# Kernel tuning notes

Hardware: AMD Instinct MI355X
Metric: run time of the kernel (lower is better)

## Reference

```python
import jax, jax.numpy as jnp
import numpy as np

N_NODES = 100000
N_EDGES = 1600000
N_GRAPHS = 1000
D_IN = 128
HID = 128
OUT = 6


def setup_inputs() -> dict:
    key = jax.random.key(0)
    ks = jax.random.split(key, 12)
    s = 1.0 / np.sqrt(HID)
    x = jax.random.normal(ks[0], (N_NODES, D_IN), dtype=jnp.float32)
    ei = jax.random.randint(ks[1], (2, N_EDGES), 0, N_NODES, dtype=jnp.int64)
    batch = jnp.sort(jax.random.randint(ks[2], (N_NODES,), 0, N_GRAPHS, dtype=jnp.int64))
    return {
        "x": x,
        "ei": ei,
        "batch": batch,
        "W1a": jax.random.normal(ks[3], (D_IN, HID), dtype=jnp.float32) * s,
        "b1a": jnp.zeros((HID,), jnp.float32),
        "W1b": jax.random.normal(ks[4], (HID, HID), dtype=jnp.float32) * s,
        "b1b": jnp.zeros((HID,), jnp.float32),
        "W2a": jax.random.normal(ks[5], (HID, HID), dtype=jnp.float32) * s,
        "b2a": jnp.zeros((HID,), jnp.float32),
        "W2b": jax.random.normal(ks[6], (HID, HID), dtype=jnp.float32) * s,
        "b2b": jnp.zeros((HID,), jnp.float32),
        "Wlin": jax.random.normal(ks[7], (HID, OUT), dtype=jnp.float32) * s,
        "blin": jnp.zeros((OUT,), jnp.float32),
    }


def _gin_conv(x, src, dst, Wa, ba, Wb, bb):
    # PyG GINConv (eps=0): mlp(x_i + sum_{j->i} x_j)
    agg = jax.ops.segment_sum(x[src], dst, num_segments=N_NODES)
    h = agg + x
    h = jnp.maximum(h @ Wa + ba, 0.0)
    return h @ Wb + bb


def reference(x, ei, batch, W1a, b1a, W1b, b1b, W2a, b2a, W2b, b2b, Wlin, blin):
    src, dst = ei[0], ei[1]
    h = jnp.maximum(_gin_conv(x, src, dst, W1a, b1a, W1b, b1b), 0.0)
    # dropout is identity in eval mode
    h = _gin_conv(h, src, dst, W2a, b2a, W2b, b2b)
    # global mean pool per graph
    sums = jax.ops.segment_sum(h, batch, num_segments=N_GRAPHS)
    cnts = jax.ops.segment_sum(jnp.ones((h.shape[0], 1), h.dtype), batch, num_segments=N_GRAPHS)
    pooled = sums / jnp.maximum(cnts, 1.0)
    return pooled @ Wlin + blin
```

## Files before the change

kernel.cpp:

```cpp
#include <hip/hip_runtime.h>

#define N_NODES 100000
#define N_EDGES 1600000
#define N_GRAPHS 1000
#define HID 128
#define OUTD 6

#define BUCK_LOG 7
#define BUCK_W (1 << BUCK_LOG)
#define NBUCK ((N_NODES + BUCK_W - 1) >> BUCK_LOG)
#define BCAP 4096
#define FILL_BLOCKS 512
#define FILL_CHUNK 3128

#define CVT_BLOCKS 6250
#define GST_BLOCKS 391
#define PACK_BLOCKS 32
#define PREP_BLOCKS (CVT_BLOCKS + GST_BLOCKS + PACK_BLOCKS + FILL_BLOCKS)

typedef _Float16 h2 __attribute__((ext_vector_type(2)));
typedef _Float16 half8 __attribute__((ext_vector_type(8)));
typedef float f32x4 __attribute__((ext_vector_type(4)));

__global__ __launch_bounds__(256) void k_prep(const float* __restrict__ x,
                                              const int* __restrict__ batch,
                                              const int* __restrict__ srcv,
                                              const int* __restrict__ dstv,
                                              const float* __restrict__ W1a,
                                              const float* __restrict__ W1b,
                                              const float* __restrict__ W2a,
                                              const float* __restrict__ W2b,
                                              _Float16* __restrict__ X16,
                                              int* __restrict__ gstart,
                                              _Float16* __restrict__ P,
                                              int* __restrict__ bcur0,
                                              int* __restrict__ packed) {
    __shared__ int h[NBUCK];
    __shared__ int lcur[NBUCK];
    int b = blockIdx.x, t = threadIdx.x;
    if (b < FILL_BLOCKS) {
        int e0 = b * FILL_CHUNK;
        int e1 = min(e0 + FILL_CHUNK, N_EDGES);
        for (int i = t; i < NBUCK; i += 256) h[i] = 0;
        __syncthreads();
        int ev = e0 + ((e1 - e0) & ~3);
        for (int e = e0 + t * 4; e < ev; e += 1024) {
            int4 d4 = *(const int4*)(dstv + e);
            atomicAdd(&h[d4.x >> BUCK_LOG], 1);
            atomicAdd(&h[d4.y >> BUCK_LOG], 1);
            atomicAdd(&h[d4.z >> BUCK_LOG], 1);
            atomicAdd(&h[d4.w >> BUCK_LOG], 1);
        }
        for (int e = ev + t; e < e1; e += 256) atomicAdd(&h[dstv[e] >> BUCK_LOG], 1);
        __syncthreads();
        for (int i = t; i < NBUCK; i += 256) {
            int c = h[i];
            lcur[i] = c ? atomicAdd(&bcur0[i], c) : 0;
        }
        __syncthreads();
        for (int e = e0 + t * 4; e < ev; e += 1024) {
            int4 d4 = *(const int4*)(dstv + e);
            int4 s4 = *(const int4*)(srcv + e);
            int b0 = d4.x >> BUCK_LOG, b1 = d4.y >> BUCK_LOG;
            int b2 = d4.z >> BUCK_LOG, b3 = d4.w >> BUCK_LOG;
            int p0 = atomicAdd(&lcur[b0], 1);
            int p1 = atomicAdd(&lcur[b1], 1);
            int p2 = atomicAdd(&lcur[b2], 1);
            int p3 = atomicAdd(&lcur[b3], 1);
            if (p0 < BCAP) packed[b0 * BCAP + p0] = ((d4.x & (BUCK_W - 1)) << 20) | s4.x;
            if (p1 < BCAP) packed[b1 * BCAP + p1] = ((d4.y & (BUCK_W - 1)) << 20) | s4.y;
            if (p2 < BCAP) packed[b2 * BCAP + p2] = ((d4.z & (BUCK_W - 1)) << 20) | s4.z;
            if (p3 < BCAP) packed[b3 * BCAP + p3] = ((d4.w & (BUCK_W - 1)) << 20) | s4.w;
        }
        for (int e = ev + t; e < e1; e += 256) {
            int d = dstv[e];
            int bk = d >> BUCK_LOG;
            int pos = atomicAdd(&lcur[bk], 1);
            if (pos < BCAP) packed[bk * BCAP + pos] = ((d & (BUCK_W - 1)) << 20) | srcv[e];
        }
    } else if (b < FILL_BLOCKS + CVT_BLOCKS) {
        size_t i = ((size_t)(b - FILL_BLOCKS) * 256 + t) * 8;
        float4 v0 = *(const float4*)(x + i);
        float4 v1 = *(const float4*)(x + i + 4);
        half8 o;
        o[0] = (_Float16)v0.x; o[1] = (_Float16)v0.y; o[2] = (_Float16)v0.z; o[3] = (_Float16)v0.w;
        o[4] = (_Float16)v1.x; o[5] = (_Float16)v1.y; o[6] = (_Float16)v1.z; o[7] = (_Float16)v1.w;
        *(half8*)(X16 + i) = o;
    } else if (b < FILL_BLOCKS + CVT_BLOCKS + GST_BLOCKS) {
        int n = (b - FILL_BLOCKS - CVT_BLOCKS) * 256 + t;
        if (n < N_NODES) {
            int bb = batch[n];
            int prev = (n == 0) ? -1 : batch[n - 1];
            for (int g = prev + 1; g <= bb; ++g) gstart[g] = n;
            if (n == N_NODES - 1)
                for (int g = bb + 1; g <= N_GRAPHS; ++g) gstart[g] = N_NODES;
        }
    } else {
        int gid = (b - FILL_BLOCKS - CVT_BLOCKS - GST_BLOCKS) * 256 + t;
        int mat = gid >> 11;
        int r = gid & 2047;
        int ctks = r >> 6;
        int lane = r & 63;
        int col = (ctks >> 2) * 16 + (lane & 15);
        int k0 = (ctks & 3) * 32 + (lane >> 4) * 8;
        const float* W = (mat == 0) ? W1a : (mat == 1) ? W1b : (mat == 2) ? W2a : W2b;
        _Float16* dp = P + mat * 16384 + r * 8;
#pragma unroll
        for (int j = 0; j < 8; ++j) dp[j] = (_Float16)W[(k0 + j) * HID + col];
    }
}

__global__ __launch_bounds__(256) void k_csrfine(const int* __restrict__ packed,
                                                 const int* __restrict__ bcur0,
                                                 int* __restrict__ offsets,
                                                 int* __restrict__ csr_src) {
    __shared__ int hist[BUCK_W];
    __shared__ int scan[BUCK_W];
    __shared__ int cur[BUCK_W];
    __shared__ int red[4];
    int b = blockIdx.x;
    int base = b << BUCK_LOG;
    int t = threadIdx.x;
    int partial = 0;
    for (int j = t; j < b; j += 256) partial += bcur0[j];
#pragma unroll
    for (int d = 32; d > 0; d >>= 1) partial += __shfl_down(partial, d, 64);
    if ((t & 63) == 0) red[t >> 6] = partial;
    __syncthreads();
    int s = red[0] + red[1] + red[2] + red[3];
    int cnt = bcur0[b];
    const int* pb = packed + b * BCAP;

    if (t < BUCK_W) hist[t] = 0;
    __syncthreads();
    for (int i = t; i < cnt; i += 256) atomicAdd(&hist[pb[i] >> 20], 1);
    __syncthreads();
    if (t < BUCK_W) scan[t] = hist[t];
    __syncthreads();
    for (int d = 1; d < BUCK_W; d <<= 1) {
        int a = 0;
        if (t >= d && t < BUCK_W) a = scan[t - d];
        __syncthreads();
        if (t < BUCK_W) scan[t] += a;
        __syncthreads();
    }
    if (t < BUCK_W) {
        int node = base + t;
        if (node < N_NODES) {
            int excl = scan[t] - hist[t];
            offsets[node] = s + excl;
            cur[t] = excl;
        }
    }
    if (b == 0 && t == 0) offsets[N_NODES] = N_EDGES;
    __syncthreads();
    for (int i = t; i < cnt; i += 256) {
        int v = pb[i];
        int ln = v >> 20;
        int pos = atomicAdd(&cur[ln], 1);
        csr_src[s + pos] = v & 0xFFFFF;
    }
}

__global__ __launch_bounds__(256) void k_gather16(const _Float16* __restrict__ x,
                                                  const int* __restrict__ csr,
                                                  const int* __restrict__ offs,
                                                  _Float16* __restrict__ out) {
    int node = __builtin_amdgcn_readfirstlane(blockIdx.x * 4 + (threadIdx.x >> 6));
    int lane = threadIdx.x & 63;
    const h2* xp = (const h2*)x;
    int s = offs[node], e = offs[node + 1];
    h2 a0 = xp[(size_t)node * 64 + lane];
    h2 z; z[0] = (_Float16)0; z[1] = (_Float16)0;
    h2 a1 = z, a2 = z, a3 = z, a4 = z, a5 = z, a6 = z, a7 = z;
    for (int base = s; base < e; base += 64) {
        int cnt = e - base;
        if (cnt > 64) cnt = 64;
        int myidx = 0;
        if (base + lane < e) myidx = csr[base + lane];
        int j = 0;
        for (; j + 8 <= cnt; j += 8) {
            int s0 = __builtin_amdgcn_readlane(myidx, j);
            int s1 = __builtin_amdgcn_readlane(myidx, j + 1);
            int s2 = __builtin_amdgcn_readlane(myidx, j + 2);
            int s3 = __builtin_amdgcn_readlane(myidx, j + 3);
            int s4 = __builtin_amdgcn_readlane(myidx, j + 4);
            int s5 = __builtin_amdgcn_readlane(myidx, j + 5);
            int s6 = __builtin_amdgcn_readlane(myidx, j + 6);
            int s7 = __builtin_amdgcn_readlane(myidx, j + 7);
            a0 += xp[(size_t)s0 * 64 + lane];
            a1 += xp[(size_t)s1 * 64 + lane];
            a2 += xp[(size_t)s2 * 64 + lane];
            a3 += xp[(size_t)s3 * 64 + lane];
            a4 += xp[(size_t)s4 * 64 + lane];
            a5 += xp[(size_t)s5 * 64 + lane];
            a6 += xp[(size_t)s6 * 64 + lane];
            a7 += xp[(size_t)s7 * 64 + lane];
        }
        for (; j + 2 <= cnt; j += 2) {
            int s0 = __builtin_amdgcn_readlane(myidx, j);
            int s1 = __builtin_amdgcn_readlane(myidx, j + 1);
            a0 += xp[(size_t)s0 * 64 + lane];
            a1 += xp[(size_t)s1 * 64 + lane];
        }
        for (; j < cnt; ++j) {
            int sc = __builtin_amdgcn_readlane(myidx, j);
            a0 += xp[(size_t)sc * 64 + lane];
        }
    }
    h2 r = ((a0 + a1) + (a2 + a3)) + ((a4 + a5) + (a6 + a7));
    ((h2*)out)[(size_t)node * 64 + lane] = r;
}

static __device__ __forceinline__ unsigned long long pack4(float v0, float v1,
                                                           float v2, float v3) {
    union { h2 h[2]; unsigned long long u; } u;
    h2 p0, p1;
    p0[0] = (_Float16)v0; p0[1] = (_Float16)v1;
    p1[0] = (_Float16)v2; p1[1] = (_Float16)v3;
    u.h[0] = p0; u.h[1] = p1;
    return u.u;
}

template <int RELU_OUT>
__global__ __launch_bounds__(256, 2) void k_mlp16(const _Float16* __restrict__ in,
                                                  const _Float16* __restrict__ Wap,
                                                  const float* __restrict__ ba,
                                                  const _Float16* __restrict__ Wbp,
                                                  const float* __restrict__ bb,
                                                  _Float16* __restrict__ out) {
    __shared__ uint4 WaS4[2048];
    __shared__ uint4 WbS4[2048];
    __shared__ unsigned long long hS[4][512];
    int t = threadIdx.x;
    int wave = t >> 6, lane = t & 63;
    int l = lane & 15, w = lane >> 4;
    int row0 = blockIdx.x * 256 + wave * 64;

    const uint4* wa4 = (const uint4*)Wap;
    const uint4* wb4 = (const uint4*)Wbp;
#pragma unroll
    for (int i = 0; i < 8; ++i) WaS4[t + i * 256] = wa4[t + i * 256];
#pragma unroll
    for (int i = 0; i < 8; ++i) WbS4[t + i * 256] = wb4[t + i * 256];
    __syncthreads();
    const half8* waf = (const half8*)WaS4;
    const half8* wbf = (const half8*)WbS4;
    unsigned long long* h64 = hS[wave];
    int swz = ((l & 3) << 2) ^ (((l >> 2) & 1) << 1);

    float4 baR[8], bbR[8];
#pragma unroll
    for (int ct = 0; ct < 8; ++ct) {
        baR[ct] = *(const float4*)(ba + ct * 16 + w * 4);
        bbR[ct] = *(const float4*)(bb + ct * 16 + w * 4);
    }

#pragma unroll
    for (int tile = 0; tile < 4; ++tile) {
        int row = row0 + tile * 16 + l;
        bool rok = row < N_NODES;
        const _Float16* rp = in + (size_t)row * HID + w * 8;
        half8 xf[4];
#pragma unroll
        for (int ks = 0; ks < 4; ++ks) {
            half8 v = {0, 0, 0, 0, 0, 0, 0, 0};
            if (rok) v = *(const half8*)(rp + ks * 32);
            xf[ks] = v;
        }
#pragma unroll
        for (int ct = 0; ct < 8; ++ct) {
            f32x4 c = {0.f, 0.f, 0.f, 0.f};
#pragma unroll
            for (int ks = 0; ks < 4; ++ks)
                c = __builtin_amdgcn_mfma_f32_16x16x32_f16(waf[(ct * 4 + ks) * 64 + lane],
                                                           xf[ks], c, 0, 0, 0);
            float4 b4 = baR[ct];
            h64[l * 32 + ((ct * 4 + w) ^ swz)] =
                pack4(fmaxf(c[0] + b4.x, 0.f), fmaxf(c[1] + b4.y, 0.f),
                      fmaxf(c[2] + b4.z, 0.f), fmaxf(c[3] + b4.w, 0.f));
        }
        half8 hf[4];
#pragma unroll
        for (int ks = 0; ks < 4; ++ks) {
            int slot = (ks * 8 + w * 2) ^ swz;
            hf[ks] = *(const half8*)&h64[l * 32 + slot];
        }
#pragma unroll
        for (int ct = 0; ct < 8; ++ct) {
            f32x4 c = {0.f, 0.f, 0.f, 0.f};
#pragma unroll
            for (int ks = 0; ks < 4; ++ks)
                c = __builtin_amdgcn_mfma_f32_16x16x32_f16(wbf[(ct * 4 + ks) * 64 + lane],
                                                           hf[ks], c, 0, 0, 0);
            float4 b4 = bbR[ct];
            float v0 = c[0] + b4.x, v1 = c[1] + b4.y, v2 = c[2] + b4.z, v3 = c[3] + b4.w;
            if (RELU_OUT) {
                v0 = fmaxf(v0, 0.f); v1 = fmaxf(v1, 0.f);
                v2 = fmaxf(v2, 0.f); v3 = fmaxf(v3, 0.f);
            }
            if (rok)
                *(unsigned long long*)(out + (size_t)row * HID + ct * 16 + w * 4) =
                    pack4(v0, v1, v2, v3);
        }
    }
}

__global__ __launch_bounds__(256) void k_pool_head(const _Float16* __restrict__ h,
                                                   const int* __restrict__ gstart,
                                                   const float* __restrict__ Wlin,
                                                   const float* __restrict__ blin,
                                                   float* __restrict__ out) {
    __shared__ float sums[4][HID];
    int g = blockIdx.x;
    int t = threadIdx.x;
    int wave = t >> 6, lane = t & 63;
    int s = gstart[g], e = gstart[g + 1];
    float ax = 0.f, ay = 0.f;
    const h2* hp = (const h2*)h;
    int r = s + wave;
    for (; r + 12 < e; r += 16) {
        h2 v0 = hp[(size_t)r * 64 + lane];
        h2 v1 = hp[(size_t)(r + 4) * 64 + lane];
        h2 v2 = hp[(size_t)(r + 8) * 64 + lane];
        h2 v3 = hp[(size_t)(r + 12) * 64 + lane];
        ax += (float)v0[0] + (float)v1[0] + (float)v2[0] + (float)v3[0];
        ay += (float)v0[1] + (float)v1[1] + (float)v2[1] + (float)v3[1];
    }
    for (; r < e; r += 4) {
        h2 v = hp[(size_t)r * 64 + lane];
        ax += (float)v[0];
        ay += (float)v[1];
    }
    sums[wave][2 * lane] = ax;
    sums[wave][2 * lane + 1] = ay;
    __syncthreads();
    if (wave != 0) return;
    float c = fmaxf((float)(e - s), 1.0f);
    float px = (sums[0][2 * lane] + sums[1][2 * lane] + sums[2][2 * lane] + sums[3][2 * lane]) / c;
    float py = (sums[0][2 * lane + 1] + sums[1][2 * lane + 1] + sums[2][2 * lane + 1] +
                sums[3][2 * lane + 1]) / c;
#pragma unroll
    for (int o = 0; o < OUTD; ++o) {
        float v = px * Wlin[(2 * lane) * OUTD + o] + py * Wlin[(2 * lane + 1) * OUTD + o];
#pragma unroll
        for (int d = 32; d > 0; d >>= 1) v += __shfl_down(v, d, 64);
        if (lane == 0) out[g * OUTD + o] = v + blin[o];
    }
}

extern "C" void kernel_launch(void* const* d_in, const int* in_sizes, int n_in,
                              void* d_out, int out_size, void* d_ws, size_t ws_size,
                              hipStream_t stream) {
    const float* x    = (const float*)d_in[0];
    const int*   ei   = (const int*)d_in[1];
    const int*   batch= (const int*)d_in[2];
    const float* W1a  = (const float*)d_in[3];
    const float* b1a  = (const float*)d_in[4];
    const float* W1b  = (const float*)d_in[5];
    const float* b1b  = (const float*)d_in[6];
    const float* W2a  = (const float*)d_in[7];
    const float* b2a  = (const float*)d_in[8];
    const float* W2b  = (const float*)d_in[9];
    const float* b2b  = (const float*)d_in[10];
    const float* Wlin = (const float*)d_in[11];
    const float* blin = (const float*)d_in[12];
    const int* src = ei;
    const int* dst = ei + N_EDGES;
    float* out = (float*)d_out;

    char* ws = (char*)d_ws;
    size_t off = 0;
    auto alloc = [&](size_t bytes) -> void* {
        void* p = ws + off;
        off += (bytes + 255) & ~(size_t)255;
        return p;
    };
    _Float16* X16 = (_Float16*)alloc(2ull * N_NODES * HID);
    _Float16* M   = (_Float16*)alloc(2ull * N_NODES * HID + 65536);
    _Float16* H1  = (_Float16*)alloc(2ull * N_NODES * HID + 65536);
    int*   csr_src = (int*)alloc(sizeof(int) * (size_t)N_EDGES);
    int*   offsets = (int*)alloc(sizeof(int) * (N_NODES + 1));
    int*   gstart  = (int*)alloc(sizeof(int) * (N_GRAPHS + 1));
    int*   bcur0   = (int*)alloc(sizeof(int) * NBUCK);
    _Float16* Wpack = (_Float16*)alloc(2ull * 4 * 16384);
    int* packed = (int*)H1;
    _Float16* M2 = M;
    _Float16* H2 = X16;
    (void)ws_size; (void)in_sizes; (void)n_in; (void)out_size;

    hipMemsetAsync(bcur0, 0, sizeof(int) * NBUCK, stream);

    k_prep<<<PREP_BLOCKS, 256, 0, stream>>>(x, batch, src, dst, W1a, W1b, W2a, W2b,
                                            X16, gstart, Wpack, bcur0, packed);
    k_csrfine<<<NBUCK, 256, 0, stream>>>(packed, bcur0, offsets, csr_src);

    k_gather16<<<N_NODES / 4, 256, 0, stream>>>(X16, csr_src, offsets, M);
    k_mlp16<1><<<(N_NODES + 255) / 256, 256, 0, stream>>>(M, Wpack + 0 * 16384, b1a,
                                                          Wpack + 1 * 16384, b1b, H1);
    k_gather16<<<N_NODES / 4, 256, 0, stream>>>(H1, csr_src, offsets, M2);
    k_mlp16<0><<<(N_NODES + 255) / 256, 256, 0, stream>>>(M2, Wpack + 2 * 16384, b2a,
                                                          Wpack + 3 * 16384, b2b, H2);

    k_pool_head<<<N_GRAPHS, 256, 0, stream>>>(H2, gstart, Wlin, blin, out);
}
```

Before: 310.3 us.

## Gather four nodes per wavefront with 16-byte half8 loads per lane

Rewrites the neighbor-sum gather so each 64-lane wave handles four nodes, with 16 lanes per node each loading a half8 (16 bytes) rather than one node per wave with h2 loads. Neighbor indices are read directly per lane, and the loop runs to the wave's maximum degree, reduced with shuffles, processing four edges per iteration into two accumulators. The aim is wider memory transactions and fewer instructions and blocks per node. In exchange, lanes diverge when the four nodes have different degrees, and fewer independent loads are in flight per node.

```diff
diff --git a/kernel.cpp b/kernel.cpp
--- a/kernel.cpp
+++ b/kernel.cpp
@@ -166,50 +166,34 @@
                                                   const int* __restrict__ csr,
                                                   const int* __restrict__ offs,
                                                   _Float16* __restrict__ out) {
-    int node = __builtin_amdgcn_readfirstlane(blockIdx.x * 4 + (threadIdx.x >> 6));
-    int lane = threadIdx.x & 63;
-    const h2* xp = (const h2*)x;
+    int t = threadIdx.x;
+    int wave = t >> 6, lane = t & 63;
+    int g = lane >> 4;
+    int l = lane & 15;
+    int node = blockIdx.x * 16 + wave * 4 + g;
+    const half8* xp8 = (const half8*)x;
     int s = offs[node], e = offs[node + 1];
-    h2 a0 = xp[(size_t)node * 64 + lane];
-    h2 z; z[0] = (_Float16)0; z[1] = (_Float16)0;
-    h2 a1 = z, a2 = z, a3 = z, a4 = z, a5 = z, a6 = z, a7 = z;
-    for (int base = s; base < e; base += 64) {
-        int cnt = e - base;
-        if (cnt > 64) cnt = 64;
-        int myidx = 0;
-        if (base + lane < e) myidx = csr[base + lane];
-        int j = 0;
-        for (; j + 8 <= cnt; j += 8) {
-            int s0 = __builtin_amdgcn_readlane(myidx, j);
-            int s1 = __builtin_amdgcn_readlane(myidx, j + 1);
-            int s2 = __builtin_amdgcn_readlane(myidx, j + 2);
-            int s3 = __builtin_amdgcn_readlane(myidx, j + 3);
-            int s4 = __builtin_amdgcn_readlane(myidx, j + 4);
-            int s5 = __builtin_amdgcn_readlane(myidx, j + 5);
-            int s6 = __builtin_amdgcn_readlane(myidx, j + 6);
-            int s7 = __builtin_amdgcn_readlane(myidx, j + 7);
-            a0 += xp[(size_t)s0 * 64 + lane];
-            a1 += xp[(size_t)s1 * 64 + lane];
-            a2 += xp[(size_t)s2 * 64 + lane];
-            a3 += xp[(size_t)s3 * 64 + lane];
-            a4 += xp[(size_t)s4 * 64 + lane];
-            a5 += xp[(size_t)s5 * 64 + lane];
-            a6 += xp[(size_t)s6 * 64 + lane];
-            a7 += xp[(size_t)s7 * 64 + lane];
-        }
-        for (; j + 2 <= cnt; j += 2) {
-            int s0 = __builtin_amdgcn_readlane(myidx, j);
-            int s1 = __builtin_amdgcn_readlane(myidx, j + 1);
-            a0 += xp[(size_t)s0 * 64 + lane];
-            a1 += xp[(size_t)s1 * 64 + lane];
-        }
-        for (; j < cnt; ++j) {
-            int sc = __builtin_amdgcn_readlane(myidx, j);
-            a0 += xp[(size_t)sc * 64 + lane];
-        }
-    }
-    h2 r = ((a0 + a1) + (a2 + a3)) + ((a4 + a5) + (a6 + a7));
-    ((h2*)out)[(size_t)node * 64 + lane] = r;
+    int cnt = e - s;
+    int mx = cnt;
+#pragma unroll
+    for (int d = 32; d > 0; d >>= 1) mx = max(mx, __shfl_xor(mx, d, 64));
+
+    half8 acc0 = xp8[(size_t)node * 16 + l];
+    half8 acc1 = {0, 0, 0, 0, 0, 0, 0, 0};
+
+    for (int it = 0; it < mx; it += 4) {
+        int p = s + it;
+        int i0 = -1, i1 = -1, i2 = -1, i3 = -1;
+        if (p + 0 < e) i0 = csr[p + 0];
+        if (p + 1 < e) i1 = csr[p + 1];
+        if (p + 2 < e) i2 = csr[p + 2];
+        if (p + 3 < e) i3 = csr[p + 3];
+        if (i0 >= 0) acc0 += xp8[(size_t)i0 * 16 + l];
+        if (i1 >= 0) acc1 += xp8[(size_t)i1 * 16 + l];
+        if (i2 >= 0) acc0 += xp8[(size_t)i2 * 16 + l];
+        if (i3 >= 0) acc1 += xp8[(size_t)i3 * 16 + l];
+    }
+    ((half8*)out)[(size_t)node * 16 + l] = acc0 + acc1;
 }
 
 static __device__ __forceinline__ unsigned long long pack4(float v0, float v1,
@@ -395,10 +379,10 @@
                                             X16, gstart, Wpack, bcur0, packed);
     k_csrfine<<<NBUCK, 256, 0, stream>>>(packed, bcur0, offsets, csr_src);
 
-    k_gather16<<<N_NODES / 4, 256, 0, stream>>>(X16, csr_src, offsets, M);
+    k_gather16<<<N_NODES / 16, 256, 0, stream>>>(X16, csr_src, offsets, M);
     k_mlp16<1><<<(N_NODES + 255) / 256, 256, 0, stream>>>(M, Wpack + 0 * 16384, b1a,
                                                           Wpack + 1 * 16384, b1b, H1);
-    k_gather16<<<N_NODES / 4, 256, 0, stream>>>(H1, csr_src, offsets, M2);
+    k_gather16<<<N_NODES / 16, 256, 0, stream>>>(H1, csr_src, offsets, M2);
     k_mlp16<0><<<(N_NODES + 255) / 256, 256, 0, stream>>>(M2, Wpack + 2 * 16384, b2a,
                                                           Wpack + 3 * 16384, b2b, H2);
 
```

Result: slower. 324.0 us (+4.4%).
